# Kernel optimization log

Measured on AMD Instinct MI355X. Metric: run time of the kernel, lower is better.

## Reference

```python
import jax, jax.numpy as jnp
import numpy as np

DEPTH = 4
HEADS = 8
DIM_HEAD = 32
NUM_CLUSTERS = 64
KMEANS_ITERS = 10
EPS = 1e-5


def layer_norm(x, g, b):
    m = jnp.mean(x, axis=-1, keepdims=True)
    v = jnp.var(x, axis=-1, keepdims=True)
    return (x - m) * jax.lax.rsqrt(v + EPS) * g + b


def kmeans_cluster(xf, k, iters):
    # xf: [P, D]. Lloyd's algorithm with deterministic init (first k points).
    centers = xf[:k]
    x_sq = jnp.sum(xf * xf, axis=-1, keepdims=True)  # [P,1]

    def assign(c):
        # squared distances [P, K]
        d = x_sq - 2.0 * (xf @ c.T) + jnp.sum(c * c, axis=-1)[None, :]
        return jnp.argmin(d, axis=-1)

    def step(c, _):
        labels = assign(c)
        sums = jax.ops.segment_sum(xf, labels, num_segments=k)
        counts = jax.ops.segment_sum(jnp.ones((xf.shape[0],), xf.dtype), labels, num_segments=k)
        new_c = jnp.where(counts[:, None] > 0, sums / jnp.maximum(counts, 1.0)[:, None], c)
        return new_c, None

    centers, _ = jax.lax.scan(step, centers, None, length=iters)
    labels = assign(centers)
    return centers[labels]  # gather: [P, D]


def setup_inputs() -> dict:
    key = jax.random.key(0)
    ks = jax.random.split(key, 8)
    B, N, D, L, M = 8, 1024, 256, DEPTH, 1024
    s = 0.02
    return {
        "x": jax.random.normal(ks[0], (B, N, D), jnp.float32),
        "ln1_g": jnp.ones((L, D), jnp.float32),
        "ln1_b": jnp.zeros((L, D), jnp.float32),
        "Wq": jax.random.normal(ks[1], (L, D, HEADS * DIM_HEAD), jnp.float32) * s,
        "Wkv": jax.random.normal(ks[2], (L, D, 2 * HEADS * DIM_HEAD), jnp.float32) * s,
        "Wo": jax.random.normal(ks[3], (L, HEADS * DIM_HEAD, D), jnp.float32) * s,
        "bo": jnp.zeros((L, D), jnp.float32),
        "ln2_g": jnp.ones((L, D), jnp.float32),
        "ln2_b": jnp.zeros((L, D), jnp.float32),
        "W1": jax.random.normal(ks[4], (L, D, M), jnp.float32) * s,
        "b1": jnp.zeros((L, M), jnp.float32),
        "W2": jax.random.normal(ks[5], (L, M, D), jnp.float32) * s,
        "b2": jnp.zeros((L, D), jnp.float32),
        "kW": jax.random.normal(ks[6], (D, D), jnp.float32) * s,
        "kb": jnp.zeros((D,), jnp.float32),
    }


def reference(x, ln1_g, ln1_b, Wq, Wkv, Wo, bo, ln2_g, ln2_b, W1, b1, W2, b2, kW, kb):
    B, N, D = x.shape
    h, dh = HEADS, DIM_HEAD
    scale = dh ** -0.5
    for l in range(DEPTH):
        # PreNorm self-attention + residual
        xn = layer_norm(x, ln1_g[l], ln1_b[l])
        q = (xn @ Wq[l]).reshape(B, N, h, dh)
        kv = xn @ Wkv[l]
        k, v = jnp.split(kv, 2, axis=-1)
        k = k.reshape(B, N, h, dh)
        v = v.reshape(B, N, h, dh)
        dots = jnp.einsum("bqhd,bkhd->bhqk", q, k) * scale
        attn = jax.nn.softmax(dots, axis=-1)
        out = jnp.einsum("bhqk,bkhd->bqhd", attn, v).reshape(B, N, h * dh)
        x = out @ Wo[l] + bo[l] + x
        # PreNorm FFN + residual
        xn = layer_norm(x, ln2_g[l], ln2_b[l])
        hdd = jax.nn.gelu(xn @ W1[l] + b1[l], approximate=False)
        x = hdd @ W2[l] + b2[l] + x
    # KMeans module: cluster flattened tokens, gather centers, linear transform.
    xf = x.reshape(B * N, D)
    clustered = kmeans_cluster(xf, NUM_CLUSTERS, KMEANS_ITERS)
    clustered = jax.lax.stop_gradient(clustered)  # torch detaches before sklearn
    clustered = clustered.reshape(B, N, D)
    return clustered @ kW + kb
```

## Files before the change

kernel.cpp:

```cpp
#include <hip/hip_runtime.h>
#include <hip/hip_bf16.h>
#include <math.h>

#define BN 8192
#define DMODEL 256
#define FFN 1024
#define NCLUST 64

typedef unsigned short u16;
typedef unsigned int u32;
typedef __attribute__((ext_vector_type(8))) short s16x8;
typedef __attribute__((ext_vector_type(8))) unsigned short u16x8;
typedef __attribute__((ext_vector_type(4))) unsigned short u16x4;
typedef __attribute__((ext_vector_type(4))) float f32x4;

__device__ __forceinline__ float bf2f(u16 v) {
    union { unsigned int u; float f; } w; w.u = ((unsigned int)v) << 16; return w.f;
}
__device__ __forceinline__ u16 f2bf(float f) {
    union { float f; unsigned int u; } w; w.f = f;
    unsigned int r = w.u + 0x7fffu + ((w.u >> 16) & 1u);
    return (u16)(r >> 16);
}
__device__ __forceinline__ u32 cvtpk(float lo, float hi) {
    u32 r;
    asm("v_cvt_pk_bf16_f32 %0, %1, %2" : "=v"(r) : "v"(lo), "v"(hi));
    return r;
}
__device__ __forceinline__ float u2f(u32 u) { union { u32 u; float f; } w; w.u = u; return w.f; }

__device__ __forceinline__ void gl16(const u16* g, u16* l) {
    __builtin_amdgcn_global_load_lds((const __attribute__((address_space(1))) u32*)g,
                                     (__attribute__((address_space(3))) u32*)l, 16, 0, 0);
}

#define BARRIER_LGKM() asm volatile("s_waitcnt lgkmcnt(0)\n\ts_barrier" ::: "memory")
#define MEMFENCE_ORDER() asm volatile("" ::: "memory")

__device__ __forceinline__ int sw32(int row, int col) { return row * 32 + (col ^ (((row >> 1) & 3) << 3)); }
__device__ __forceinline__ int sw64(int row, int col) { return row * 64 + (col ^ ((row & 7) << 3)); }
template<int BK>
__device__ __forceinline__ int swk(int row, int col) {
    if constexpr (BK == 32) return row * 32 + (col ^ (((row >> 1) & 3) << 3));
    else                    return row * 64 + (col ^ ((row & 7) << 3));
}

__global__ __launch_bounds__(256) void ln_wave(const float* __restrict__ x, const float* __restrict__ g,
                                               const float* __restrict__ b, u16* __restrict__ yh,
                                               u16* __restrict__ yl) {
    int t = threadIdx.x, w = t >> 6, l = t & 63;
    int row = blockIdx.x * 4 + w;
    const float* xr = x + (size_t)row * DMODEL;
    float4 v = *reinterpret_cast<const float4*>(xr + l * 4);
    float s = v.x + v.y + v.z + v.w;
    for (int off = 1; off < 64; off <<= 1) s += __shfl_xor(s, off);
    float mean = s * (1.0f / 256.0f);
    float4 dv = make_float4(v.x - mean, v.y - mean, v.z - mean, v.w - mean);
    float vs = dv.x * dv.x + dv.y * dv.y + dv.z * dv.z + dv.w * dv.w;
    for (int off = 1; off < 64; off <<= 1) vs += __shfl_xor(vs, off);
    float rs = rsqrtf(vs * (1.0f / 256.0f) + 1e-5f);
    float4 gg = *reinterpret_cast<const float4*>(g + l * 4);
    float4 bb = *reinterpret_cast<const float4*>(b + l * 4);
    float os[4] = {dv.x * rs * gg.x + bb.x, dv.y * rs * gg.y + bb.y,
                   dv.z * rs * gg.z + bb.z, dv.w * rs * gg.w + bb.w};
    u16x4 hv, lv;
#pragma unroll
    for (int j = 0; j < 4; j++) { u16 hh = f2bf(os[j]); hv[j] = hh; lv[j] = f2bf(os[j] - bf2f(hh)); }
    size_t o = (size_t)row * DMODEL + l * 4;
    *reinterpret_cast<u16x4*>(yh + o) = hv;
    *reinterpret_cast<u16x4*>(yl + o) = lv;
}

__device__ __forceinline__ void wconv_body(const float* __restrict__ W, u16* __restrict__ th,
                                           u16* __restrict__ tl, int K, int N, int bx, int by) {
    __shared__ float T[64][65];
    int k0 = by * 64, n0 = bx * 64;
    int t = threadIdx.x;
    int r = t >> 4, c4 = (t & 15) * 4;
#pragma unroll
    for (int i = 0; i < 4; i++) {
        float4 x = *reinterpret_cast<const float4*>(W + (size_t)(k0 + r + 16 * i) * N + n0 + c4);
        T[r + 16 * i][c4] = x.x; T[r + 16 * i][c4 + 1] = x.y;
        T[r + 16 * i][c4 + 2] = x.z; T[r + 16 * i][c4 + 3] = x.w;
    }
    __syncthreads();
#pragma unroll
    for (int i = 0; i < 4; i++) {
        int n = r + 16 * i;
        u16x4 h4, l4;
#pragma unroll
        for (int j = 0; j < 4; j++) {
            float v = T[c4 + j][n];
            u16 h = f2bf(v);
            h4[j] = h; l4[j] = f2bf(v - bf2f(h));
        }
        *reinterpret_cast<u16x4*>(th + (size_t)(n0 + n) * K + k0 + c4) = h4;
        *reinterpret_cast<u16x4*>(tl + (size_t)(n0 + n) * K + k0 + c4) = l4;
    }
}

__global__ __launch_bounds__(256) void wconv_all(const float* __restrict__ Wq, const float* __restrict__ Wkv,
                                                 const float* __restrict__ Wo, const float* __restrict__ W1,
                                                 const float* __restrict__ W2,
                                                 u16* __restrict__ wqkvh, u16* __restrict__ wqkvl,
                                                 u16* __restrict__ woh, u16* __restrict__ wol,
                                                 u16* __restrict__ w1h, u16* __restrict__ w1l,
                                                 u16* __restrict__ w2h, u16* __restrict__ w2l) {
    int f = blockIdx.x;
    if (f < 16)       wconv_body(Wq,  wqkvh,               wqkvl,               256, 256,  f & 3,  f >> 2);
    else if (f < 48)  { int g = f - 16;  wconv_body(Wkv, wqkvh + 65536,       wqkvl + 65536,       256, 512,  g & 7,  g >> 3); }
    else if (f < 64)  { int g = f - 48;  wconv_body(Wo,  woh,                 wol,                 256, 256,  g & 3,  g >> 2); }
    else if (f < 128) { int g = f - 64;  wconv_body(W1,  w1h,                 w1l,                 256, 1024, g & 15, g >> 4); }
    else              { int g = f - 128; wconv_body(W2,  w2h,                 w2l,                 1024, 256, g & 3,  g >> 2); }
}

template<int BM, int BNT, int BK>
__global__ __launch_bounds__(256) void gemm_t(const u16* __restrict__ Ath, const u16* __restrict__ Atl,
                                              const u16* __restrict__ Bth, const u16* __restrict__ Btl,
                                              const float* __restrict__ bias, const float* __restrict__ resid,
                                              float* __restrict__ Cf, u16* __restrict__ Ch, u16* __restrict__ Cl,
                                              int M, int N, int K, int fuse_gelu) {
    __shared__ u16 Ah[2][BM * BK], Al[2][BM * BK];
    __shared__ u16 Bh[2][BNT * BK], Bl[2][BNT * BK];
    constexpr int WAVES_N = (BM == 128 && BNT == 64) ? 1 : 2;
    constexpr int WAVES_M = 4 / WAVES_N;
    constexpr int MI = BM / (16 * WAVES_M);
    constexpr int NI = BNT / (16 * WAVES_N);
    constexpr int SEGS = (BM + BNT) * BK / 1024;
    constexpr int ROWS_SEG = 512 / BK;
    constexpr int ASEG = BM / ROWS_SEG;
    constexpr int BSEG = BNT / ROWS_SEG;
    int t = threadIdx.x;
    int gx = gridDim.x;
    int nwg = gx * gridDim.y;
    int lin = blockIdx.y * gx + blockIdx.x;
    int swz = (lin & 7) * (nwg >> 3) + (lin >> 3);
    int bx = swz % gx, by = swz / gx;
    int m0 = by * BM, n0 = bx * BNT;
    int L = t & 63, w = t >> 6, fr = L & 15, quad = L >> 4;
    int wm = (WAVES_N == 1) ? w : (w & 1);
    int wn = (WAVES_N == 1) ? 0 : (w >> 1);

    const u16* gsrc[SEGS];
    u16* ldst[SEGS];
    u32 dlt[SEGS];
    {
        int lr, lc;
        if constexpr (BK == 32) { lr = L >> 2; lc = (L & 3) * 8; }
        else                    { lr = L >> 3; lc = (L & 7) * 8; }
#pragma unroll
        for (int i = 0; i < SEGS; i++) {
            int s = w * SEGS + i;
            const u16* gb; u16* lb; int r; u32 d;
            if (s < ASEG)                 { gb = Ath + (size_t)m0 * K; lb = &Ah[0][0]; r = s * ROWS_SEG;                 d = BM * BK; }
            else if (s < 2 * ASEG)        { gb = Atl + (size_t)m0 * K; lb = &Al[0][0]; r = (s - ASEG) * ROWS_SEG;        d = BM * BK; }
            else if (s < 2 * ASEG + BSEG) { gb = Bth + (size_t)n0 * K; lb = &Bh[0][0]; r = (s - 2 * ASEG) * ROWS_SEG;    d = BNT * BK; }
            else                          { gb = Btl + (size_t)n0 * K; lb = &Bl[0][0]; r = (s - 2 * ASEG - BSEG) * ROWS_SEG; d = BNT * BK; }
            int row = r + lr;
            int scol;
            if constexpr (BK == 32) scol = lc ^ (((row >> 1) & 3) << 3);
            else                    scol = lc ^ ((row & 7) << 3);
            gsrc[i] = gb + (size_t)row * K + scol;
            ldst[i] = lb + r * BK;
            dlt[i] = d;
        }
    }

    f32x4 acc[MI][NI];
#pragma unroll
    for (int i = 0; i < MI; i++)
#pragma unroll
        for (int j = 0; j < NI; j++) acc[i][j] = (f32x4){0.0f, 0.0f, 0.0f, 0.0f};

    const int NT = K / BK;
#pragma unroll
    for (int i = 0; i < SEGS; i++) gl16(gsrc[i], ldst[i]);

    for (int tt = 0; tt < NT; tt++) {
        asm volatile("s_waitcnt lgkmcnt(0)" ::: "memory");
        __builtin_amdgcn_s_barrier();
        if (tt + 1 < NT) {
            int k0n = (tt + 1) * BK;
            u32 sel = (u32)((tt + 1) & 1);
#pragma unroll
            for (int i = 0; i < SEGS; i++) gl16(gsrc[i] + k0n, ldst[i] + sel * dlt[i]);
            asm volatile("s_waitcnt vmcnt(%0)" :: "n"(SEGS) : "memory");
        } else {
            asm volatile("s_waitcnt vmcnt(0)" ::: "memory");
        }
        __builtin_amdgcn_s_barrier();
        __builtin_amdgcn_sched_barrier(0);
        int cb = tt & 1;
        const u16* AhB = &Ah[cb][0]; const u16* AlB = &Al[cb][0];
        const u16* BhB = &Bh[cb][0]; const u16* BlB = &Bl[cb][0];
#pragma unroll
        for (int kk = 0; kk < BK / 32; kk++) {
            int kc = kk * 32 + quad * 8;
            s16x8 ah[MI], al[MI];
#pragma unroll
            for (int mi = 0; mi < MI; mi++) {
                int row = wm * (MI * 16) + mi * 16 + fr;
                ah[mi] = *reinterpret_cast<const s16x8*>(&AhB[swk<BK>(row, kc)]);
                al[mi] = *reinterpret_cast<const s16x8*>(&AlB[swk<BK>(row, kc)]);
            }
            __builtin_amdgcn_s_setprio(1);
#pragma unroll
            for (int ni = 0; ni < NI; ni++) {
                int rn = wn * (NI * 16) + ni * 16 + fr;
                s16x8 bhf = *reinterpret_cast<const s16x8*>(&BhB[swk<BK>(rn, kc)]);
                s16x8 blf = *reinterpret_cast<const s16x8*>(&BlB[swk<BK>(rn, kc)]);
#pragma unroll
                for (int mi = 0; mi < MI; mi++) {
                    acc[mi][ni] = __builtin_amdgcn_mfma_f32_16x16x32_bf16(ah[mi], bhf, acc[mi][ni], 0, 0, 0);
                    acc[mi][ni] = __builtin_amdgcn_mfma_f32_16x16x32_bf16(ah[mi], blf, acc[mi][ni], 0, 0, 0);
                    acc[mi][ni] = __builtin_amdgcn_mfma_f32_16x16x32_bf16(al[mi], bhf, acc[mi][ni], 0, 0, 0);
                }
            }
            __builtin_amdgcn_s_setprio(0);
        }
    }
#pragma unroll
    for (int mi = 0; mi < MI; mi++) {
#pragma unroll
        for (int ni = 0; ni < NI; ni++) {
#pragma unroll
            for (int r = 0; r < 4; r++) {
                int row = m0 + wm * (MI * 16) + mi * 16 + quad * 4 + r;
                int col = n0 + wn * (NI * 16) + ni * 16 + fr;
                float v = acc[mi][ni][r];
                if (bias) v += bias[col];
                if (fuse_gelu) v = 0.5f * v * (1.0f + erff(v * 0.70710678118654752f));
                if (resid) v += resid[(size_t)row * N + col];
                size_t o = (size_t)row * N + col;
                if (Cf) Cf[o] = v;
                if (Ch) { u16 hh = f2bf(v); Ch[o] = hh; Cl[o] = f2bf(v - bf2f(hh)); }
            }
        }
    }
}

__global__ __launch_bounds__(256) void attn14(const u16* __restrict__ qkvh, const u16* __restrict__ qkvl,
                                              u16* __restrict__ aoh, u16* __restrict__ aol) {
    int bh = blockIdx.x, b = bh >> 3, h = bh & 7;
    int qt = blockIdx.y;
    int t = threadIdx.x, L = t & 63, w = t >> 6;
    int fr = L & 15, quad = L >> 4;
    __shared__ u16 KH[2][64 * 32], KL[2][64 * 32];
    __shared__ u16 VTH[32 * 64], VTL[32 * 64];
    __shared__ u16 PH[4][16 * 64], PL[4][16 * 64];
    const float scale = 0.17677669529663687f;
    const int ROWS = 768;

    const u16* ksrc[2];
    u16* kdst[2];
    {
        int lr = L >> 2, lc = (L & 3) * 8;
#pragma unroll
        for (int i = 0; i < 2; i++) {
            int s = w * 2 + i;
            const u16* gb = (s < 4) ? qkvh : qkvl;
            u16* lb = (s < 4) ? &KH[0][0] : &KL[0][0];
            int r = (s & 3) * 16;
            int row = r + lr;
            int scol = lc ^ (((row >> 1) & 3) << 3);
            ksrc[i] = gb + ((size_t)(b * 1024) + row) * ROWS + 256 + h * 32 + scol;
            kdst[i] = lb + r * 32;
        }
    }

    size_t qoff0 = (size_t)(b * 1024 + qt * 128 + w * 16 + fr) * ROWS + h * 32 + quad * 8;
    s16x8 aqh0 = *reinterpret_cast<const s16x8*>(qkvh + qoff0);
    s16x8 aql0 = *reinterpret_cast<const s16x8*>(qkvl + qoff0);
    s16x8 aqh1 = *reinterpret_cast<const s16x8*>(qkvh + qoff0 + (size_t)64 * ROWS);
    s16x8 aql1 = *reinterpret_cast<const s16x8*>(qkvl + qoff0 + (size_t)64 * ROWS);

    int vp = t >> 3, vd0 = (t & 7) * 4;
    const u16* vh_ptr = qkvh + (size_t)(b * 1024 + 2 * vp) * ROWS + 512 + h * 32 + vd0;
    const u16* vl_ptr = qkvl + (size_t)(b * 1024 + 2 * vp) * ROWS + 512 + h * 32 + vd0;
    u16x4 vh0, vh1, vl0, vl1;
#define LOADV(kt_) do { size_t o_ = (size_t)((kt_) * 64) * ROWS;                                  \
        vh0 = *reinterpret_cast<const u16x4*>(vh_ptr + o_);                                       \
        vh1 = *reinterpret_cast<const u16x4*>(vh_ptr + o_ + ROWS);                                \
        vl0 = *reinterpret_cast<const u16x4*>(vl_ptr + o_);                                       \
        vl1 = *reinterpret_cast<const u16x4*>(vl_ptr + o_ + ROWS); } while (0)

    gl16(ksrc[0], kdst[0]);
    gl16(ksrc[1], kdst[1]);
    MEMFENCE_ORDER();
    LOADV(0);

    float m_0 = -1e30f, l_0 = 0.0f, m_1 = -1e30f, l_1 = 0.0f;
    f32x4 accA0, accA1, accB0, accB1;
    accA0 = (f32x4){0.0f, 0.0f, 0.0f, 0.0f}; accA1 = accA0; accB0 = accA0; accB1 = accA0;

#define SM_PV(SV, M_I, L_I, ACC0, ACC1) do {                                                      \
        float p[16];                                                                              \
        float ml = -1e30f;                                                                        \
        _Pragma("unroll")                                                                         \
        for (int ni = 0; ni < 4; ni++)                                                            \
            _Pragma("unroll")                                                                     \
            for (int r = 0; r < 4; r++) { float v = SV[ni][r] * scale; p[ni * 4 + r] = v; ml = fmaxf(ml, v); } \
        ml = fmaxf(ml, __shfl_xor(ml, 16));                                                       \
        ml = fmaxf(ml, __shfl_xor(ml, 32));                                                       \
        float mnew = fmaxf(M_I, ml);                                                              \
        float alpha = __expf(M_I - mnew);                                                         \
        M_I = mnew;                                                                               \
        float rs = 0.0f;                                                                          \
        _Pragma("unroll")                                                                         \
        for (int i = 0; i < 16; i++) { float e = __expf(p[i] - mnew); p[i] = e; rs += e; }        \
        rs += __shfl_xor(rs, 16);                                                                 \
        rs += __shfl_xor(rs, 32);                                                                 \
        L_I = L_I * alpha + rs;                                                                   \
        _Pragma("unroll")                                                                         \
        for (int ni = 0; ni < 4; ni++) {                                                          \
            float p0 = p[ni * 4], p1 = p[ni * 4 + 1], p2 = p[ni * 4 + 2], p3 = p[ni * 4 + 3];     \
            u32 qh01 = cvtpk(p0, p1), qh23 = cvtpk(p2, p3);                                       \
            float e0 = p0 - u2f(qh01 << 16);                                                      \
            float e1 = p1 - u2f(qh01 & 0xffff0000u);                                              \
            float e2 = p2 - u2f(qh23 << 16);                                                      \
            float e3 = p3 - u2f(qh23 & 0xffff0000u);                                              \
            u32 ql01 = cvtpk(e0, e1), ql23 = cvtpk(e2, e3);                                       \
            int c0 = sw64(fr, ni * 16 + quad * 4);                                                \
            int c1 = sw64(fr, ni * 16 + quad * 4 + 2);                                            \
            *reinterpret_cast<u32*>(&PH[w][c0]) = qh01;                                           \
            *reinterpret_cast<u32*>(&PH[w][c1]) = qh23;                                           \
            *reinterpret_cast<u32*>(&PL[w][c0]) = ql01;                                           \
            *reinterpret_cast<u32*>(&PL[w][c1]) = ql23;                                           \
        }                                                                                         \
        float a4[4];                                                                              \
        _Pragma("unroll")                                                                         \
        for (int r = 0; r < 4; r++) a4[r] = __shfl(alpha, quad * 4 + r);                          \
        ACC0[0] *= a4[0]; ACC0[1] *= a4[1]; ACC0[2] *= a4[2]; ACC0[3] *= a4[3];                   \
        ACC1[0] *= a4[0]; ACC1[1] *= a4[1]; ACC1[2] *= a4[2]; ACC1[3] *= a4[3];                   \
        __builtin_amdgcn_s_setprio(1);                                                            \
        _Pragma("unroll")                                                                         \
        for (int ks = 0; ks < 2; ks++) {                                                          \
            s16x8 aph = *reinterpret_cast<s16x8*>(&PH[w][sw64(fr, ks * 32 + quad * 8)]);          \
            s16x8 apl = *reinterpret_cast<s16x8*>(&PL[w][sw64(fr, ks * 32 + quad * 8)]);          \
            s16x8 bvh0 = *reinterpret_cast<s16x8*>(&VTH[sw64(fr, ks * 32 + quad * 8)]);           \
            s16x8 bvl0 = *reinterpret_cast<s16x8*>(&VTL[sw64(fr, ks * 32 + quad * 8)]);           \
            ACC0 = __builtin_amdgcn_mfma_f32_16x16x32_bf16(aph, bvh0, ACC0, 0, 0, 0);             \
            ACC0 = __builtin_amdgcn_mfma_f32_16x16x32_bf16(aph, bvl0, ACC0, 0, 0, 0);             \
            ACC0 = __builtin_amdgcn_mfma_f32_16x16x32_bf16(apl, bvh0, ACC0, 0, 0, 0);             \
            s16x8 bvh1 = *reinterpret_cast<s16x8*>(&VTH[sw64(16 + fr, ks * 32 + quad * 8)]);      \
            s16x8 bvl1 = *reinterpret_cast<s16x8*>(&VTL[sw64(16 + fr, ks * 32 + quad * 8)]);      \
            ACC1 = __builtin_amdgcn_mfma_f32_16x16x32_bf16(aph, bvh1, ACC1, 0, 0, 0);             \
            ACC1 = __builtin_amdgcn_mfma_f32_16x16x32_bf16(aph, bvl1, ACC1, 0, 0, 0);             \
            ACC1 = __builtin_amdgcn_mfma_f32_16x16x32_bf16(apl, bvh1, ACC1, 0, 0, 0);             \
        }                                                                                         \
        __builtin_amdgcn_s_setprio(0);                                                            \
    } while (0)

#pragma unroll 2
    for (int kt = 0; kt < 16; kt++) {
        int cur = kt & 1;
        BARRIER_LGKM();
        if (kt < 15) {
            size_t koff = (size_t)((kt + 1) * 64) * ROWS;
            u32 sel = (u32)((kt + 1) & 1) * (64 * 32);
            gl16(ksrc[0] + koff, kdst[0] + sel);
            gl16(ksrc[1] + koff, kdst[1] + sel);
        }
        {
#pragma unroll
            for (int i = 0; i < 4; i++) {
                int idx = sw64(vd0 + i, 2 * vp);
                *reinterpret_cast<u32*>(&VTH[idx]) = (u32)vh0[i] | ((u32)vh1[i] << 16);
                *reinterpret_cast<u32*>(&VTL[idx]) = (u32)vl0[i] | ((u32)vl1[i] << 16);
            }
        }
        BARRIER_LGKM();
        f32x4 sv0[4], sv1[4];
        __builtin_amdgcn_s_setprio(1);
#pragma unroll
        for (int ni = 0; ni < 4; ni++) {
            s16x8 bkh = *reinterpret_cast<s16x8*>(&KH[cur][sw32(ni * 16 + fr, quad * 8)]);
            s16x8 bkl = *reinterpret_cast<s16x8*>(&KL[cur][sw32(ni * 16 + fr, quad * 8)]);
            f32x4 c0 = (f32x4){0.0f, 0.0f, 0.0f, 0.0f};
            c0 = __builtin_amdgcn_mfma_f32_16x16x32_bf16(bkh, aqh0, c0, 0, 0, 0);
            c0 = __builtin_amdgcn_mfma_f32_16x16x32_bf16(bkl, aqh0, c0, 0, 0, 0);
            c0 = __builtin_amdgcn_mfma_f32_16x16x32_bf16(bkh, aql0, c0, 0, 0, 0);
            sv0[ni] = c0;
            f32x4 c1 = (f32x4){0.0f, 0.0f, 0.0f, 0.0f};
            c1 = __builtin_amdgcn_mfma_f32_16x16x32_bf16(bkh, aqh1, c1, 0, 0, 0);
            c1 = __builtin_amdgcn_mfma_f32_16x16x32_bf16(bkl, aqh1, c1, 0, 0, 0);
            c1 = __builtin_amdgcn_mfma_f32_16x16x32_bf16(bkh, aql1, c1, 0, 0, 0);
            sv1[ni] = c1;
        }
        __builtin_amdgcn_s_setprio(0);
        if (kt < 15) LOADV(kt + 1);
        SM_PV(sv0, m_0, l_0, accA0, accA1);
        SM_PV(sv1, m_1, l_1, accB0, accB1);
    }
#undef SM_PV
#undef LOADV
    float invl0 = 1.0f / l_0, invl1 = 1.0f / l_1;
#pragma unroll
    for (int r = 0; r < 4; r++) {
        float iv0 = __shfl(invl0, quad * 4 + r);
        float iv1 = __shfl(invl1, quad * 4 + r);
        size_t rb0 = ((size_t)(b * 1024 + qt * 128 + w * 16 + quad * 4 + r)) * DMODEL + h * 32;
        size_t rb1 = rb0 + (size_t)64 * DMODEL;
        float v0 = accA0[r] * iv0, v1 = accA1[r] * iv0;
        u16 h0 = f2bf(v0); aoh[rb0 + fr] = h0;      aol[rb0 + fr] = f2bf(v0 - bf2f(h0));
        u16 h1 = f2bf(v1); aoh[rb0 + 16 + fr] = h1; aol[rb0 + 16 + fr] = f2bf(v1 - bf2f(h1));
        float v2 = accB0[r] * iv1, v3 = accB1[r] * iv1;
        u16 h2 = f2bf(v2); aoh[rb1 + fr] = h2;      aol[rb1 + fr] = f2bf(v2 - bf2f(h2));
        u16 h3 = f2bf(v3); aoh[rb1 + 16 + fr] = h3; aol[rb1 + 16 + fr] = f2bf(v3 - bf2f(h3));
    }
}

__global__ __launch_bounds__(64) void csq_k(const float* __restrict__ centers, float* __restrict__ csq) {
    int j = blockIdx.x, l = threadIdx.x;
    float4 c4 = *reinterpret_cast<const float4*>(centers + j * DMODEL + l * 4);
    float s = c4.x * c4.x + c4.y * c4.y + c4.z * c4.z + c4.w * c4.w;
    for (int off = 1; off < 64; off <<= 1) s += __shfl_xor(s, off);
    if (l == 0) csq[j] = s;
}

__global__ __launch_bounds__(256) void km_distmin(const float* __restrict__ A, const float* __restrict__ Cn,
                                                  const float* __restrict__ csq, int* __restrict__ labels) {
    __shared__ float Cs[256][68];
    int t = threadIdx.x, tx = t & 15, ty = t >> 4;
    int m0 = blockIdx.x * 16;
    {
        int j = t & 63, kc = (t >> 6) * 64;
#pragma unroll
        for (int i = 0; i < 16; i++) {
            float4 c4 = *reinterpret_cast<const float4*>(Cn + (size_t)j * DMODEL + kc + i * 4);
            Cs[kc + i * 4 + 0][j] = c4.x; Cs[kc + i * 4 + 1][j] = c4.y;
            Cs[kc + i * 4 + 2][j] = c4.z; Cs[kc + i * 4 + 3][j] = c4.w;
        }
    }
    __syncthreads();
    const float* ar = A + (size_t)(m0 + ty) * DMODEL;
    float acc[4] = {};
    for (int kb = 0; kb < 64; kb++) {
        float4 a4 = *reinterpret_cast<const float4*>(ar + kb * 4);
        float4 b0 = *reinterpret_cast<float4*>(&Cs[kb * 4 + 0][tx * 4]);
        float4 b1 = *reinterpret_cast<float4*>(&Cs[kb * 4 + 1][tx * 4]);
        float4 b2 = *reinterpret_cast<float4*>(&Cs[kb * 4 + 2][tx * 4]);
        float4 b3 = *reinterpret_cast<float4*>(&Cs[kb * 4 + 3][tx * 4]);
        acc[0] += a4.x * b0.x; acc[1] += a4.x * b0.y; acc[2] += a4.x * b0.z; acc[3] += a4.x * b0.w;
        acc[0] += a4.y * b1.x; acc[1] += a4.y * b1.y; acc[2] += a4.y * b1.z; acc[3] += a4.y * b1.w;
        acc[0] += a4.z * b2.x; acc[1] += a4.z * b2.y; acc[2] += a4.z * b2.z; acc[3] += a4.z * b2.w;
        acc[0] += a4.w * b3.x; acc[1] += a4.w * b3.y; acc[2] += a4.w * b3.z; acc[3] += a4.w * b3.w;
    }
    float4 cs4 = *reinterpret_cast<const float4*>(csq + tx * 4);
    float csv[4] = {cs4.x, cs4.y, cs4.z, cs4.w};
    float best = csv[0] - 2.0f * acc[0]; int bi = tx * 4;
#pragma unroll
    for (int j = 1; j < 4; j++) {
        float v = csv[j] - 2.0f * acc[j];
        if (v < best) { best = v; bi = tx * 4 + j; }
    }
    for (int off = 1; off < 16; off <<= 1) {
        float ov = __shfl_xor(best, off);
        int oi = __shfl_xor(bi, off);
        if (ov < best || (ov == best && oi < bi)) { best = ov; bi = oi; }
    }
    if (tx == 0) labels[m0 + ty] = bi;
}

__global__ __launch_bounds__(256) void km_segsum(const int* __restrict__ labels, const float* __restrict__ xf,
                                                 float* __restrict__ sums16, float* __restrict__ counts16) {
    int c = blockIdx.x, j = blockIdx.y, t = threadIdx.x;
    __shared__ int labs[512];
    if (t < 128) {
        int4 l4 = *reinterpret_cast<const int4*>(labels + c * 512 + t * 4);
        labs[t * 4] = l4.x; labs[t * 4 + 1] = l4.y; labs[t * 4 + 2] = l4.z; labs[t * 4 + 3] = l4.w;
    }
    __syncthreads();
    float acc = 0.0f, cnt = 0.0f;
    const float* xb = xf + (size_t)c * 512 * DMODEL;
    for (int i = 0; i < 512; i++) {
        if (labs[i] == j) { acc += xb[(size_t)i * DMODEL + t]; cnt += 1.0f; }
    }
    sums16[((size_t)c * NCLUST + j) * DMODEL + t] = acc;
    if (t == 0) counts16[c * NCLUST + j] = cnt;
}

__global__ __launch_bounds__(256) void km_update(float* __restrict__ centers, const float* __restrict__ sums16,
                                                 const float* __restrict__ counts16, float* __restrict__ csq) {
    __shared__ float red[256];
    int j = blockIdx.x, d = threadIdx.x;
    float c = 0.0f;
#pragma unroll
    for (int cc = 0; cc < 16; cc++) c += counts16[cc * NCLUST + j];
    float sv = 0.0f;
#pragma unroll
    for (int cc = 0; cc < 16; cc++) sv += sums16[((size_t)cc * NCLUST + j) * DMODEL + d];
    float cv = centers[j * DMODEL + d];
    if (c > 0.0f) cv = sv / fmaxf(c, 1.0f);
    centers[j * DMODEL + d] = cv;
    red[d] = cv * cv;
    __syncthreads();
    for (int off = 128; off; off >>= 1) { if (d < off) red[d] += red[d + off]; __syncthreads(); }
    if (d == 0) csq[j] = red[0];
}

__global__ __launch_bounds__(256) void nproj(const float* __restrict__ centers, const float* __restrict__ kW,
                                             const float* __restrict__ kb2, float* __restrict__ outc) {
    int idx = blockIdx.x * 256 + threadIdx.x;
    if (idx >= NCLUST * DMODEL) return;
    int row = idx >> 8, col = idx & 255;
    const float* cr = centers + row * DMODEL;
    float acc = 0.0f;
    for (int d = 0; d < DMODEL; d++) acc += cr[d] * kW[(size_t)d * DMODEL + col];
    outc[idx] = acc + kb2[col];
}

__global__ __launch_bounds__(256) void km_gather(const int* __restrict__ labels, const float* __restrict__ outc,
                                                 float* __restrict__ out) {
    int t = threadIdx.x;
#pragma unroll
    for (int r = 0; r < 4; r++) {
        int i = blockIdx.x * 4 + r;
        int lab = labels[i];
        out[(size_t)i * DMODEL + t] = outc[lab * DMODEL + t];
    }
}

extern "C" void kernel_launch(void* const* d_in, const int* in_sizes, int n_in,
                              void* d_out, int out_size, void* d_ws, size_t ws_size,
                              hipStream_t stream) {
    const float* x_in  = (const float*)d_in[0];
    const float* ln1_g = (const float*)d_in[1];
    const float* ln1_b = (const float*)d_in[2];
    const float* Wq    = (const float*)d_in[3];
    const float* Wkv   = (const float*)d_in[4];
    const float* Wo    = (const float*)d_in[5];
    const float* bo    = (const float*)d_in[6];
    const float* ln2_g = (const float*)d_in[7];
    const float* ln2_b = (const float*)d_in[8];
    const float* W1    = (const float*)d_in[9];
    const float* b1    = (const float*)d_in[10];
    const float* W2    = (const float*)d_in[11];
    const float* b2    = (const float*)d_in[12];
    const float* kWp   = (const float*)d_in[13];
    const float* kbp   = (const float*)d_in[14];
    float* out = (float*)d_out;

    const size_t NEEDED = 53477376;
    if (ws_size < NEEDED) {
        hipMemsetAsync(d_out, 0, (size_t)out_size * sizeof(float), stream);
        return;
    }

    char* ws = (char*)d_ws;
    float* xf      = (float*)(ws);
    u16*   xnh     = (u16*)  (ws + 8388608);
    u16*   xnl     = (u16*)  (ws + 12582912);
    u16*   aoh     = xnh;
    u16*   aol     = xnl;
    u16*   qkvh    = (u16*)  (ws + 16777216);
    u16*   qkvl    = (u16*)  (ws + 29360128);
    u16*   hbh     = (u16*)  (ws + 16777216);
    u16*   hbl     = (u16*)  (ws + 33554432);
    float* centers = (float*)(ws + 41943040);
    float* csqb    = (float*)(ws + 42008576);
    float* counts16= (float*)(ws + 42008832);
    int*   labels  = (int*)  (ws + 42012928);
    float* outc    = (float*)(ws + 42045696);
    float* sums16  = (float*)(ws + 42111232);
    u16*   wr      = (u16*)  (ws + 50331648);
    u16 *wqkvh = wr,          *wqkvl = wr + 196608;
    u16 *woh = wr + 393216,   *wol = wr + 458752;
    u16 *w1h = wr + 524288,   *w1l = wr + 786432;
    u16 *w2h = wr + 1048576,  *w2l = wr + 1310720;

    hipMemcpyAsync(xf, x_in, (size_t)BN * DMODEL * sizeof(float), hipMemcpyDeviceToDevice, stream);

    for (int l = 0; l < 4; l++) {
        wconv_all<<<192, 256, 0, stream>>>(Wq + (size_t)l * 65536, Wkv + (size_t)l * 131072,
                                           Wo + (size_t)l * 65536, W1 + (size_t)l * 262144,
                                           W2 + (size_t)l * 262144,
                                           wqkvh, wqkvl, woh, wol, w1h, w1l, w2h, w2l);

        ln_wave<<<BN / 4, 256, 0, stream>>>(xf, ln1_g + l * 256, ln1_b + l * 256, xnh, xnl);
        gemm_t<128, 128, 32><<<dim3(6, 64), 256, 0, stream>>>(xnh, xnl, wqkvh, wqkvl, nullptr, nullptr,
                                                              nullptr, qkvh, qkvl, BN, 768, 256, 0);
        attn14<<<dim3(64, 8), 256, 0, stream>>>(qkvh, qkvl, aoh, aol);
        gemm_t<64, 64, 64><<<dim3(4, 128), 256, 0, stream>>>(aoh, aol, woh, wol, bo + l * 256, xf,
                                                             xf, nullptr, nullptr, BN, 256, 256, 0);
        ln_wave<<<BN / 4, 256, 0, stream>>>(xf, ln2_g + l * 256, ln2_b + l * 256, xnh, xnl);
        gemm_t<128, 128, 32><<<dim3(8, 64), 256, 0, stream>>>(xnh, xnl, w1h, w1l, b1 + l * 1024, nullptr,
                                                              nullptr, hbh, hbl, BN, 1024, 256, 1);
        gemm_t<64, 64, 64><<<dim3(4, 128), 256, 0, stream>>>(hbh, hbl, w2h, w2l, b2 + l * 256, xf,
                                                             xf, nullptr, nullptr, BN, 256, 1024, 0);
    }

    hipMemcpyAsync(centers, xf, NCLUST * DMODEL * sizeof(float), hipMemcpyDeviceToDevice, stream);
    csq_k<<<64, 64, 0, stream>>>(centers, csqb);
    for (int it = 0; it < 10; it++) {
        km_distmin<<<512, 256, 0, stream>>>(xf, centers, csqb, labels);
        km_segsum<<<dim3(16, NCLUST), 256, 0, stream>>>(labels, xf, sums16, counts16);
        km_update<<<64, 256, 0, stream>>>(centers, sums16, counts16, csqb);
    }
    km_distmin<<<512, 256, 0, stream>>>(xf, centers, csqb, labels);
    nproj<<<64, 256, 0, stream>>>(centers, kWp, kbp, outc);
    km_gather<<<BN / 4, 256, 0, stream>>>(labels, outc, out);
}
```

Measured before the change: 1.226 ms.

## Double rows per distmin block and split segsum into 32 chunks

```diff
diff --git a/kernel.cpp b/kernel.cpp
--- a/kernel.cpp
+++ b/kernel.cpp
@@ -422,7 +422,7 @@
                                                   const float* __restrict__ csq, int* __restrict__ labels) {
     __shared__ float Cs[256][68];
     int t = threadIdx.x, tx = t & 15, ty = t >> 4;
-    int m0 = blockIdx.x * 16;
+    int m0 = blockIdx.x * 32;
     {
         int j = t & 63, kc = (t >> 6) * 64;
 #pragma unroll
@@ -433,63 +433,85 @@
         }
     }
     __syncthreads();
-    const float* ar = A + (size_t)(m0 + ty) * DMODEL;
-    float acc[4] = {};
+    const float* ar0 = A + (size_t)(m0 + ty) * DMODEL;
+    const float* ar1 = A + (size_t)(m0 + 16 + ty) * DMODEL;
+    float acc0[4] = {}, acc1[4] = {};
     for (int kb = 0; kb < 64; kb++) {
-        float4 a4 = *reinterpret_cast<const float4*>(ar + kb * 4);
+        float4 a0 = *reinterpret_cast<const float4*>(ar0 + kb * 4);
+        float4 a1 = *reinterpret_cast<const float4*>(ar1 + kb * 4);
         float4 b0 = *reinterpret_cast<float4*>(&Cs[kb * 4 + 0][tx * 4]);
         float4 b1 = *reinterpret_cast<float4*>(&Cs[kb * 4 + 1][tx * 4]);
         float4 b2 = *reinterpret_cast<float4*>(&Cs[kb * 4 + 2][tx * 4]);
         float4 b3 = *reinterpret_cast<float4*>(&Cs[kb * 4 + 3][tx * 4]);
-        acc[0] += a4.x * b0.x; acc[1] += a4.x * b0.y; acc[2] += a4.x * b0.z; acc[3] += a4.x * b0.w;
-        acc[0] += a4.y * b1.x; acc[1] += a4.y * b1.y; acc[2] += a4.y * b1.z; acc[3] += a4.y * b1.w;
-        acc[0] += a4.z * b2.x; acc[1] += a4.z * b2.y; acc[2] += a4.z * b2.z; acc[3] += a4.z * b2.w;
-        acc[0] += a4.w * b3.x; acc[1] += a4.w * b3.y; acc[2] += a4.w * b3.z; acc[3] += a4.w * b3.w;
+        acc0[0] += a0.x * b0.x; acc0[1] += a0.x * b0.y; acc0[2] += a0.x * b0.z; acc0[3] += a0.x * b0.w;
+        acc0[0] += a0.y * b1.x; acc0[1] += a0.y * b1.y; acc0[2] += a0.y * b1.z; acc0[3] += a0.y * b1.w;
+        acc0[0] += a0.z * b2.x; acc0[1] += a0.z * b2.y; acc0[2] += a0.z * b2.z; acc0[3] += a0.z * b2.w;
+        acc0[0] += a0.w * b3.x; acc0[1] += a0.w * b3.y; acc0[2] += a0.w * b3.z; acc0[3] += a0.w * b3.w;
+        acc1[0] += a1.x * b0.x; acc1[1] += a1.x * b0.y; acc1[2] += a1.x * b0.z; acc1[3] += a1.x * b0.w;
+        acc1[0] += a1.y * b1.x; acc1[1] += a1.y * b1.y; acc1[2] += a1.y * b1.z; acc1[3] += a1.y * b1.w;
+        acc1[0] += a1.z * b2.x; acc1[1] += a1.z * b2.y; acc1[2] += a1.z * b2.z; acc1[3] += a1.z * b2.w;
+        acc1[0] += a1.w * b3.x; acc1[1] += a1.w * b3.y; acc1[2] += a1.w * b3.z; acc1[3] += a1.w * b3.w;
     }
     float4 cs4 = *reinterpret_cast<const float4*>(csq + tx * 4);
     float csv[4] = {cs4.x, cs4.y, cs4.z, cs4.w};
-    float best = csv[0] - 2.0f * acc[0]; int bi = tx * 4;
-#pragma unroll
-    for (int j = 1; j < 4; j++) {
-        float v = csv[j] - 2.0f * acc[j];
-        if (v < best) { best = v; bi = tx * 4 + j; }
-    }
-    for (int off = 1; off < 16; off <<= 1) {
-        float ov = __shfl_xor(best, off);
-        int oi = __shfl_xor(bi, off);
-        if (ov < best || (ov == best && oi < bi)) { best = ov; bi = oi; }
-    }
-    if (tx == 0) labels[m0 + ty] = bi;
+    {
+        float best = csv[0] - 2.0f * acc0[0]; int bi = tx * 4;
+#pragma unroll
+        for (int j = 1; j < 4; j++) {
+            float v = csv[j] - 2.0f * acc0[j];
+            if (v < best) { best = v; bi = tx * 4 + j; }
+        }
+        for (int off = 1; off < 16; off <<= 1) {
+            float ov = __shfl_xor(best, off);
+            int oi = __shfl_xor(bi, off);
+            if (ov < best || (ov == best && oi < bi)) { best = ov; bi = oi; }
+        }
+        if (tx == 0) labels[m0 + ty] = bi;
+    }
+    {
+        float best = csv[0] - 2.0f * acc1[0]; int bi = tx * 4;
+#pragma unroll
+        for (int j = 1; j < 4; j++) {
+            float v = csv[j] - 2.0f * acc1[j];
+            if (v < best) { best = v; bi = tx * 4 + j; }
+        }
+        for (int off = 1; off < 16; off <<= 1) {
+            float ov = __shfl_xor(best, off);
+            int oi = __shfl_xor(bi, off);
+            if (ov < best || (ov == best && oi < bi)) { best = ov; bi = oi; }
+        }
+        if (tx == 0) labels[m0 + 16 + ty] = bi;
+    }
 }
 
 __global__ __launch_bounds__(256) void km_segsum(const int* __restrict__ labels, const float* __restrict__ xf,
-                                                 float* __restrict__ sums16, float* __restrict__ counts16) {
+                                                 float* __restrict__ sums32, float* __restrict__ counts32) {
     int c = blockIdx.x, j = blockIdx.y, t = threadIdx.x;
-    __shared__ int labs[512];
-    if (t < 128) {
-        int4 l4 = *reinterpret_cast<const int4*>(labels + c * 512 + t * 4);
+    __shared__ int labs[256];
+    if (t < 64) {
+        int4 l4 = *reinterpret_cast<const int4*>(labels + c * 256 + t * 4);
         labs[t * 4] = l4.x; labs[t * 4 + 1] = l4.y; labs[t * 4 + 2] = l4.z; labs[t * 4 + 3] = l4.w;
     }
     __syncthreads();
     float acc = 0.0f, cnt = 0.0f;
-    const float* xb = xf + (size_t)c * 512 * DMODEL;
-    for (int i = 0; i < 512; i++) {
+    const float* xb = xf + (size_t)c * 256 * DMODEL;
+    for (int i = 0; i < 256; i++) {
         if (labs[i] == j) { acc += xb[(size_t)i * DMODEL + t]; cnt += 1.0f; }
     }
-    sums16[((size_t)c * NCLUST + j) * DMODEL + t] = acc;
-    if (t == 0) counts16[c * NCLUST + j] = cnt;
-}
-
-__global__ __launch_bounds__(256) void km_update(float* __restrict__ centers, const float* __restrict__ sums16,
-                                                 const float* __restrict__ counts16, float* __restrict__ csq) {
+    sums32[((size_t)c * NCLUST + j) * DMODEL + t] = acc;
+    if (t == 0) counts32[c * NCLUST + j] = cnt;
+}
+
+__global__ __launch_bounds__(256) void km_update(float* __restrict__ centers, const float* __restrict__ sums32,
+                                                 const float* __restrict__ counts32, float* __restrict__ csq) {
     __shared__ float red[256];
     int j = blockIdx.x, d = threadIdx.x;
     float c = 0.0f;
 #pragma unroll
-    for (int cc = 0; cc < 16; cc++) c += counts16[cc * NCLUST + j];
+    for (int cc = 0; cc < 32; cc++) c += counts32[cc * NCLUST + j];
     float sv = 0.0f;
 #pragma unroll
-    for (int cc = 0; cc < 16; cc++) sv += sums16[((size_t)cc * NCLUST + j) * DMODEL + d];
+    for (int cc = 0; cc < 32; cc++) sv += sums32[((size_t)cc * NCLUST + j) * DMODEL + d];
     float cv = centers[j * DMODEL + d];
     if (c > 0.0f) cv = sv / fmaxf(c, 1.0f);
     centers[j * DMODEL + d] = cv;
@@ -559,10 +581,10 @@
     u16*   hbl     = (u16*)  (ws + 33554432);
     float* centers = (float*)(ws + 41943040);
     float* csqb    = (float*)(ws + 42008576);
-    float* counts16= (float*)(ws + 42008832);
-    int*   labels  = (int*)  (ws + 42012928);
-    float* outc    = (float*)(ws + 42045696);
-    float* sums16  = (float*)(ws + 42111232);
+    float* counts32= (float*)(ws + 42008832);
+    int*   labels  = (int*)  (ws + 42017024);
+    float* outc    = (float*)(ws + 42049792);
+    float* sums32  = (float*)(ws + 42115328);
     u16*   wr      = (u16*)  (ws + 50331648);
     u16 *wqkvh = wr,          *wqkvl = wr + 196608;
     u16 *woh = wr + 393216,   *wol = wr + 458752;
@@ -593,11 +615,11 @@
     hipMemcpyAsync(centers, xf, NCLUST * DMODEL * sizeof(float), hipMemcpyDeviceToDevice, stream);
     csq_k<<<64, 64, 0, stream>>>(centers, csqb);
     for (int it = 0; it < 10; it++) {
-        km_distmin<<<512, 256, 0, stream>>>(xf, centers, csqb, labels);
-        km_segsum<<<dim3(16, NCLUST), 256, 0, stream>>>(labels, xf, sums16, counts16);
-        km_update<<<64, 256, 0, stream>>>(centers, sums16, counts16, csqb);
-    }
-    km_distmin<<<512, 256, 0, stream>>>(xf, centers, csqb, labels);
+        km_distmin<<<256, 256, 0, stream>>>(xf, centers, csqb, labels);
+        km_segsum<<<dim3(32, NCLUST), 256, 0, stream>>>(labels, xf, sums32, counts32);
+        km_update<<<64, 256, 0, stream>>>(centers, sums32, counts32, csqb);
+    }
+    km_distmin<<<256, 256, 0, stream>>>(xf, centers, csqb, labels);
     nproj<<<64, 256, 0, stream>>>(centers, kWp, kbp, outc);
     km_gather<<<BN / 4, 256, 0, stream>>>(labels, outc, out);
 }
```

Measured after the change: 1.076 ms (median of 2 runs). 1.14x faster.
